# Performance work log

Measured on AMD Instinct MI355X. Metric: run time of the kernel, lower is better.

Reference implementation:

```python
import jax, jax.numpy as jnp
import numpy as np

B, T, N, D = 8, 64, 128, 128  # batch, timesteps, num_nodes, hidden_dim
LN_EPS = 1e-5
L2_EPS = 1e-12


def setup_inputs() -> dict:
    key = jax.random.key(0)
    ks = jax.random.split(key, 8)
    feat = jax.random.normal(ks[0], (B, T, N, D), dtype=jnp.float32)
    w = jax.random.uniform(ks[1], (D,), dtype=jnp.float32)  # learned adj gate (torch.rand init)
    s = 1.0 / np.sqrt(D)
    W1 = jax.random.uniform(ks[2], (D, D), dtype=jnp.float32, minval=-s, maxval=s)
    b1 = jax.random.uniform(ks[3], (D,), dtype=jnp.float32, minval=-s, maxval=s)
    W2 = jax.random.uniform(ks[4], (D, D), dtype=jnp.float32, minval=-s, maxval=s)
    b2 = jax.random.uniform(ks[5], (D,), dtype=jnp.float32, minval=-s, maxval=s)
    gamma = jnp.ones((D,), dtype=jnp.float32)
    beta = jnp.zeros((D,), dtype=jnp.float32)
    return {"feat": feat, "w": w, "W1": W1, "b1": b1, "W2": W2, "b2": b2,
            "gamma": gamma, "beta": beta}


def _windows(x):
    # x: (B, T, N, D) -> (B, T-2, 3*N, D): 3 consecutive timesteps flattened over nodes
    b, t, n, d = x.shape
    return jnp.stack([x[:, i:i + t - 2] for i in range(3)], axis=2).reshape(b, t - 2, 3 * n, d)


def reference(feat, w, W1, b1, W2, b2, gamma, beta):
    # gated + L2-normalized features for learned adjacency
    wf = feat * jax.nn.sigmoid(w)
    wf = wf / jnp.maximum(jnp.linalg.norm(wf, axis=-1, keepdims=True), L2_EPS)

    win = _windows(feat)   # (B, T-2, 3N, D)
    wwin = _windows(wf)    # (B, T-2, 3N, D)

    # learned adjacency: gram matrix per window, (B, T-2, 3N, 3N)
    adj = jnp.einsum('btmd,btnd->btmn', wwin, wwin)

    # symmetric normalization D^{-1/2} A D^{-1/2}; inf/nan (deg<=0) -> 0 as in torch
    deg = adj.sum(axis=-1, keepdims=True)
    dis = jnp.where(deg > 0, jax.lax.rsqrt(jnp.maximum(deg, 1e-38)), 0.0)
    nadj = dis * adj * jnp.swapaxes(dis, -1, -2)

    # message passing, keep last N rows (current timestep)
    agg = jnp.einsum('btmn,btnd->btmd', nadj, win)[:, :, -N:, :]

    # FFN (dropout is identity in eval): Linear -> ReLU -> Linear
    h = jax.nn.relu(agg @ W1 + b1) @ W2 + b2

    # residual with current-timestep features + LayerNorm
    s = feat[:, 2:] + h
    mu = s.mean(axis=-1, keepdims=True)
    var = ((s - mu) ** 2).mean(axis=-1, keepdims=True)
    return (s - mu) * jax.lax.rsqrt(var + LN_EPS) * gamma + beta
```

## Files before the change

### kernel.cpp

```cpp
#include <hip/hip_runtime.h>
#include <math.h>

#define BB    8
#define TDIM  64
#define NN    128
#define DD    128
#define TTOUT 62
#define W3    384
#define LG    136
#define LP    40
#define LW    72

typedef __attribute__((ext_vector_type(8))) short bf16x8;
typedef __attribute__((ext_vector_type(4))) float f32x4;

__device__ __forceinline__ float sigf(float x){ return 1.0f/(1.0f+__expf(-x)); }
__device__ __forceinline__ unsigned short f2bf(float x){
  union{float f; unsigned u;} v; v.f=x;
  unsigned r = v.u + 0x7FFFu + ((v.u>>16)&1u);
  return (unsigned short)(r>>16);
}

__global__ void k_rscale(const float* __restrict__ feat, const float* __restrict__ w,
                         float* __restrict__ rscale){
  int row  = blockIdx.x*4 + (threadIdx.x>>6);
  int lane = threadIdx.x & 63;
  float2 f  = *(const float2*)(feat + (size_t)row*DD + lane*2);
  float2 wv = *(const float2*)(w + lane*2);
  float v0 = f.x * sigf(wv.x);
  float v1 = f.y * sigf(wv.y);
  float ss = v0*v0 + v1*v1;
  #pragma unroll
  for(int k=32;k>=1;k>>=1) ss += __shfl_xor(ss, k);
  if(lane==0) rscale[row] = 1.0f / fmaxf(sqrtf(ss), 1e-12f);
}

__global__ void k_ssum(const float* __restrict__ feat, const float* __restrict__ w,
                       const float* __restrict__ rscale, float* __restrict__ ssum){
  int bt = blockIdx.x;
  int d  = threadIdx.x;
  const float* fp = feat + (size_t)bt*NN*DD + d;
  const float* rp = rscale + bt*NN;
  float acc = 0.f;
  #pragma unroll 4
  for(int n=0;n<NN;n++) acc += fp[(size_t)n*DD] * rp[n];
  ssum[bt*DD + d] = acc * sigf(w[d]);
}

__global__ void k_dis(const float* __restrict__ feat, const float* __restrict__ w,
                      const float* __restrict__ rscale, const float* __restrict__ ssum,
                      float* __restrict__ dis){
  __shared__ float s3[DD];
  __shared__ float sg[DD];
  int bt2 = blockIdx.x;
  int b = bt2 / TTOUT, tt = bt2 % TTOUT;
  int tid = threadIdx.x;
  if(tid < DD){
    int base = (b*TDIM + tt)*DD;
    s3[tid] = ssum[base+tid] + ssum[base+DD+tid] + ssum[base+2*DD+tid];
    sg[tid] = sigf(w[tid]);
  }
  __syncthreads();
  int gr = (b*TDIM + tt)*NN + tid;
  const float4* fr = (const float4*)(feat + (size_t)gr*DD);
  float deg = 0.f;
  #pragma unroll 8
  for(int q=0;q<DD/4;q++){
    float4 f = fr[q];
    deg += f.x*sg[q*4+0]*s3[q*4+0] + f.y*sg[q*4+1]*s3[q*4+1]
         + f.z*sg[q*4+2]*s3[q*4+2] + f.w*sg[q*4+3]*s3[q*4+3];
  }
  deg *= rscale[gr];
  dis[(size_t)bt2*W3 + tid] = (deg > 0.f) ? rsqrtf(fmaxf(deg, 1e-38f)) : 0.f;
}

__global__ __launch_bounds__(512,4) void k_main(
    const float* __restrict__ feat,
    const float* __restrict__ W1, const float* __restrict__ b1,
    const float* __restrict__ W2, const float* __restrict__ b2,
    const float* __restrict__ gamma, const float* __restrict__ beta,
    const float* __restrict__ w,
    const float* __restrict__ rscale, const float* __restrict__ dis,
    float* __restrict__ out)
{
  __shared__ __align__(16) unsigned short sm[32000];
  __shared__ float sSig[DD];
  unsigned short* sA  = sm;
  unsigned short* sG  = sm + 17408;
  unsigned short* sFt = sm + 21760;
  unsigned short* sP  = sm + 26880;
  unsigned short* sWt = sm + 17408;

  const int bt2 = blockIdx.x;
  const int tid = threadIdx.x;
  const int rowBase = (bt2/TTOUT)*TDIM*NN + (bt2%TTOUT)*NN;
  const float* disP = dis + (size_t)bt2*W3;

  const int lane = tid & 63, wid = tid >> 6;
  const int l15 = lane & 15, l4 = lane >> 4;
  const int m0 = wid * 16;

  if(tid < DD) sSig[tid] = sigf(w[tid]);
  __syncthreads();

  #pragma unroll
  for(int e0=0; e0<8; ++e0){
    int e = e0*512 + tid;
    int d = e & 127, r0 = (e>>7)*4;
    float sg = sSig[d];
    #pragma unroll
    for(int i=0;i<4;i++){
      int j = 256 + r0 + i, gr = rowBase + j;
      float f = feat[(size_t)gr*DD + d];
      float fac = rscale[gr]*disP[j];
      sA[(r0+i)*LG + d] = f2bf(f*sg*fac);
    }
  }

  f32x4 acc2[8];
  #pragma unroll
  for(int i=0;i<8;i++) acc2[i] = (f32x4){0.f,0.f,0.f,0.f};

  for(int c=0; c<12; ++c){
    const int n0 = c*32;
    __syncthreads();
    #pragma unroll
    for(int e0=0; e0<2; ++e0){
      int e = e0*512 + tid;
      int d = e & 127, r0 = (e>>7)*4;
      float sg = sSig[d];
      unsigned short fb[4];
      #pragma unroll
      for(int i=0;i<4;i++){
        int j = n0 + r0 + i, gr = rowBase + j;
        float f = feat[(size_t)gr*DD + d];
        float fac = rscale[gr]*disP[j];
        fb[i] = f2bf(f);
        sG[(r0+i)*LG + d] = f2bf(f*sg*fac);
      }
      unsigned int* fp = (unsigned int*)&sFt[d*LP + r0];
      fp[0] = (unsigned)fb[0] | ((unsigned)fb[1]<<16);
      fp[1] = (unsigned)fb[2] | ((unsigned)fb[3]<<16);
    }
    __syncthreads();

    f32x4 p0 = {0.f,0.f,0.f,0.f}, p1 = {0.f,0.f,0.f,0.f};
    #pragma unroll
    for(int ks=0; ks<4; ++ks){
      bf16x8 aA  = *(const bf16x8*)&sA[(m0+l15)*LG + ks*32 + l4*8];
      bf16x8 bg0 = *(const bf16x8*)&sG[( 0+l15)*LG + ks*32 + l4*8];
      bf16x8 bg1 = *(const bf16x8*)&sG[(16+l15)*LG + ks*32 + l4*8];
      p0 = __builtin_amdgcn_mfma_f32_16x16x32_bf16(aA, bg0, p0, 0,0,0);
      p1 = __builtin_amdgcn_mfma_f32_16x16x32_bf16(aA, bg1, p1, 0,0,0);
    }
    #pragma unroll
    for(int r=0;r<4;r++){
      sP[(m0 + l4*4 + r)*LP +  0 + l15] = f2bf(p0[r]);
      sP[(m0 + l4*4 + r)*LP + 16 + l15] = f2bf(p1[r]);
    }
    __syncthreads();

    bf16x8 aP = *(const bf16x8*)&sP[(m0+l15)*LP + l4*8];
    #pragma unroll
    for(int dt=0; dt<8; ++dt){
      bf16x8 bF = *(const bf16x8*)&sFt[(dt*16+l15)*LP + l4*8];
      acc2[dt] = __builtin_amdgcn_mfma_f32_16x16x32_bf16(aP, bF, acc2[dt], 0,0,0);
    }
  }

  #pragma unroll
  for(int dt=0; dt<8; ++dt)
    #pragma unroll
    for(int r=0;r<4;r++)
      sA[(m0+l4*4+r)*LG + dt*16+l15] = f2bf(acc2[dt][r]);

  f32x4 acch[8];
  #pragma unroll
  for(int dt=0; dt<8; ++dt){
    float bv = b1[dt*16+l15];
    acch[dt] = (f32x4){bv,bv,bv,bv};
  }
  for(int kh=0; kh<2; ++kh){
    __syncthreads();
    #pragma unroll
    for(int e0=0; e0<4; ++e0){
      int e = e0*512+tid;
      int n = e&127, k0 = (e>>7)*4;
      float w0 = W1[(size_t)(kh*64+k0+0)*DD + n];
      float w1v= W1[(size_t)(kh*64+k0+1)*DD + n];
      float w2v= W1[(size_t)(kh*64+k0+2)*DD + n];
      float w3v= W1[(size_t)(kh*64+k0+3)*DD + n];
      unsigned int* wp = (unsigned int*)&sWt[n*LW + k0];
      wp[0] = (unsigned)f2bf(w0) | ((unsigned)f2bf(w1v)<<16);
      wp[1] = (unsigned)f2bf(w2v)| ((unsigned)f2bf(w3v)<<16);
    }
    __syncthreads();
    #pragma unroll
    for(int ks=0; ks<2; ++ks){
      bf16x8 aA = *(const bf16x8*)&sA[(m0+l15)*LG + kh*64 + ks*32 + l4*8];
      #pragma unroll
      for(int dt=0; dt<8; ++dt){
        bf16x8 bW = *(const bf16x8*)&sWt[(dt*16+l15)*LW + ks*32 + l4*8];
        acch[dt] = __builtin_amdgcn_mfma_f32_16x16x32_bf16(aA, bW, acch[dt], 0,0,0);
      }
    }
  }
  __syncthreads();
  #pragma unroll
  for(int dt=0; dt<8; ++dt)
    #pragma unroll
    for(int r=0;r<4;r++)
      sA[(m0+l4*4+r)*LG + dt*16+l15] = f2bf(fmaxf(acch[dt][r], 0.f));

  f32x4 acco[8];
  #pragma unroll
  for(int dt=0; dt<8; ++dt){
    float bv = b2[dt*16+l15];
    acco[dt] = (f32x4){bv,bv,bv,bv};
  }
  for(int kh=0; kh<2; ++kh){
    __syncthreads();
    #pragma unroll
    for(int e0=0; e0<4; ++e0){
      int e = e0*512+tid;
      int n = e&127, k0 = (e>>7)*4;
      float w0 = W2[(size_t)(kh*64+k0+0)*DD + n];
      float w1v= W2[(size_t)(kh*64+k0+1)*DD + n];
      float w2v= W2[(size_t)(kh*64+k0+2)*DD + n];
      float w3v= W2[(size_t)(kh*64+k0+3)*DD + n];
      unsigned int* wp = (unsigned int*)&sWt[n*LW + k0];
      wp[0] = (unsigned)f2bf(w0) | ((unsigned)f2bf(w1v)<<16);
      wp[1] = (unsigned)f2bf(w2v)| ((unsigned)f2bf(w3v)<<16);
    }
    __syncthreads();
    #pragma unroll
    for(int ks=0; ks<2; ++ks){
      bf16x8 aA = *(const bf16x8*)&sA[(m0+l15)*LG + kh*64 + ks*32 + l4*8];
      #pragma unroll
      for(int dt=0; dt<8; ++dt){
        bf16x8 bW = *(const bf16x8*)&sWt[(dt*16+l15)*LW + ks*32 + l4*8];
        acco[dt] = __builtin_amdgcn_mfma_f32_16x16x32_bf16(aA, bW, acco[dt], 0,0,0);
      }
    }
  }

  const float* fres = feat + (size_t)(rowBase + 256)*DD;
  #pragma unroll
  for(int r=0;r<4;r++){
    int m = m0 + l4*4 + r;
    float vals[8]; float s1 = 0.f, s2 = 0.f;
    #pragma unroll
    for(int dt=0; dt<8; ++dt){
      int d = dt*16 + l15;
      float v = acco[dt][r] + fres[(size_t)m*DD + d];
      vals[dt] = v; s1 += v; s2 += v*v;
    }
    #pragma unroll
    for(int k=1;k<16;k<<=1){ s1 += __shfl_xor(s1,k); s2 += __shfl_xor(s2,k); }
    float mu   = s1*(1.0f/DD);
    float rstd = rsqrtf(s2*(1.0f/DD) - mu*mu + 1e-5f);
    #pragma unroll
    for(int dt=0; dt<8; ++dt){
      int d = dt*16 + l15;
      out[((size_t)bt2*NN + m)*DD + d] = (vals[dt]-mu)*rstd*gamma[d] + beta[d];
    }
  }
}

extern "C" void kernel_launch(void* const* d_in, const int* in_sizes, int n_in,
                              void* d_out, int out_size, void* d_ws, size_t ws_size,
                              hipStream_t stream){
  const float* feat  = (const float*)d_in[0];
  const float* w     = (const float*)d_in[1];
  const float* W1    = (const float*)d_in[2];
  const float* b1    = (const float*)d_in[3];
  const float* W2    = (const float*)d_in[4];
  const float* b2    = (const float*)d_in[5];
  const float* gamma = (const float*)d_in[6];
  const float* beta  = (const float*)d_in[7];
  float* out = (float*)d_out;

  float* rscale = (float*)d_ws;
  float* ssum   = rscale + BB*TDIM*NN;
  float* dis    = ssum   + BB*TDIM*DD;

  k_rscale<<<BB*TDIM*NN/4, 256, 0, stream>>>(feat, w, rscale);
  k_ssum  <<<BB*TDIM,      128, 0, stream>>>(feat, w, rscale, ssum);
  k_dis   <<<BB*TTOUT,     W3,  0, stream>>>(feat, w, rscale, ssum, dis);
  k_main  <<<BB*TTOUT,     512, 0, stream>>>(feat, W1, b1, W2, b2, gamma, beta, w,
                                             rscale, dis, out);
}
```

Baseline: 90.92 us.

## Fuse prepass kernels, pretranspose weights, double-buffer adjacency chunks in main kernel

Merges the row-norm and column-sum kernels into one pass that also converts W1/W2 into transposed bf16 copies, removing one launch and repeated weight conversion in every block. The main kernel now keeps the current-timestep A tile in registers, caches per-row scale factors in shared memory, and double-buffers the 32-row chunks with register prefetch of the next chunk's features, which cuts one barrier per iteration. It also remaps block IDs for locality and tightens shared-memory padding. The cost is higher register pressure and a heavier shuffle-reduction in the prepass.

```diff
diff --git a/kernel.cpp b/kernel.cpp
--- a/kernel.cpp
+++ b/kernel.cpp
@@ -7,9 +7,10 @@
 #define DD    128
 #define TTOUT 62
 #define W3    384
-#define LG    136
-#define LP    40
-#define LW    72
+#define LA    132
+#define LGS   132
+#define LF    36
+#define LWT   68
 
 typedef __attribute__((ext_vector_type(8))) short bf16x8;
 typedef __attribute__((ext_vector_type(4))) float f32x4;
@@ -21,30 +22,58 @@
   return (unsigned short)(r>>16);
 }
 
-__global__ void k_rscale(const float* __restrict__ feat, const float* __restrict__ w,
-                         float* __restrict__ rscale){
-  int row  = blockIdx.x*4 + (threadIdx.x>>6);
-  int lane = threadIdx.x & 63;
-  float2 f  = *(const float2*)(feat + (size_t)row*DD + lane*2);
-  float2 wv = *(const float2*)(w + lane*2);
-  float v0 = f.x * sigf(wv.x);
-  float v1 = f.y * sigf(wv.y);
-  float ss = v0*v0 + v1*v1;
-  #pragma unroll
-  for(int k=32;k>=1;k>>=1) ss += __shfl_xor(ss, k);
-  if(lane==0) rscale[row] = 1.0f / fmaxf(sqrtf(ss), 1e-12f);
-}
-
-__global__ void k_ssum(const float* __restrict__ feat, const float* __restrict__ w,
-                       const float* __restrict__ rscale, float* __restrict__ ssum){
-  int bt = blockIdx.x;
-  int d  = threadIdx.x;
-  const float* fp = feat + (size_t)bt*NN*DD + d;
-  const float* rp = rscale + bt*NN;
-  float acc = 0.f;
-  #pragma unroll 4
-  for(int n=0;n<NN;n++) acc += fp[(size_t)n*DD] * rp[n];
-  ssum[bt*DD + d] = acc * sigf(w[d]);
+__global__ __launch_bounds__(512) void k_pre(const float* __restrict__ feat,
+    const float* __restrict__ w, const float* __restrict__ W1, const float* __restrict__ W2,
+    float* __restrict__ rscale, float* __restrict__ ssum,
+    unsigned short* __restrict__ W1T, unsigned short* __restrict__ W2T){
+  __shared__ float sSig[DD];
+  __shared__ float sPart[8*DD];
+  const int bid = blockIdx.x, tid = threadIdx.x;
+  if(bid >= BB*TDIM){
+    const float* W = (bid == BB*TDIM) ? W1 : W2;
+    unsigned short* WT = (bid == BB*TDIM) ? W1T : W2T;
+    for(int e=tid; e<DD*DD; e+=512){
+      int k = e>>7, n = e&127;
+      WT[n*DD + k] = f2bf(W[(size_t)k*DD + n]);
+    }
+    return;
+  }
+  const int bt = bid;
+  if(tid < DD) sSig[tid] = sigf(w[tid]);
+  __syncthreads();
+  const int row = tid >> 2, q = tid & 3;
+  const float* fp = feat + ((size_t)bt*NN + row)*DD + q*32;
+  float g[32];
+  #pragma unroll
+  for(int i=0;i<8;i++){
+    float4 v = *(const float4*)(fp + i*4);
+    g[i*4]=v.x; g[i*4+1]=v.y; g[i*4+2]=v.z; g[i*4+3]=v.w;
+  }
+  float ss = 0.f;
+  #pragma unroll
+  for(int j=0;j<32;j++){ g[j] *= sSig[q*32+j]; ss += g[j]*g[j]; }
+  ss += __shfl_xor(ss,1); ss += __shfl_xor(ss,2);
+  float rs = 1.0f / fmaxf(sqrtf(ss), 1e-12f);
+  if(q==0) rscale[(size_t)bt*NN + row] = rs;
+  #pragma unroll
+  for(int j=0;j<32;j++) g[j] *= rs;
+  #pragma unroll
+  for(int k=4;k<64;k<<=1){
+    #pragma unroll
+    for(int j=0;j<32;j++) g[j] += __shfl_xor(g[j], k);
+  }
+  const int lane = tid & 63, wid = tid >> 6;
+  if((lane>>2)==0){
+    #pragma unroll
+    for(int j=0;j<32;j++) sPart[wid*DD + q*32 + j] = g[j];
+  }
+  __syncthreads();
+  if(tid < DD){
+    float s = 0.f;
+    #pragma unroll
+    for(int wv=0; wv<8; wv++) s += sPart[wv*DD + tid];
+    ssum[(size_t)bt*DD + tid] = s;
+  }
 }
 
 __global__ void k_dis(const float* __restrict__ feat, const float* __restrict__ w,
@@ -75,170 +104,197 @@
 }
 
 __global__ __launch_bounds__(512,4) void k_main(
-    const float* __restrict__ feat,
-    const float* __restrict__ W1, const float* __restrict__ b1,
-    const float* __restrict__ W2, const float* __restrict__ b2,
+    const float* __restrict__ feat, const float* __restrict__ w,
+    const float* __restrict__ rscale, const float* __restrict__ dis,
+    const unsigned short* __restrict__ W1T, const float* __restrict__ b1,
+    const unsigned short* __restrict__ W2T, const float* __restrict__ b2,
     const float* __restrict__ gamma, const float* __restrict__ beta,
-    const float* __restrict__ w,
-    const float* __restrict__ rscale, const float* __restrict__ dis,
     float* __restrict__ out)
 {
-  __shared__ __align__(16) unsigned short sm[32000];
-  __shared__ float sSig[DD];
-  unsigned short* sA  = sm;
-  unsigned short* sG  = sm + 17408;
-  unsigned short* sFt = sm + 21760;
-  unsigned short* sP  = sm + 26880;
-  unsigned short* sWt = sm + 17408;
-
-  const int bt2 = blockIdx.x;
-  const int tid = threadIdx.x;
-  const int rowBase = (bt2/TTOUT)*TDIM*NN + (bt2%TTOUT)*NN;
-  const float* disP = dis + (size_t)bt2*W3;
+  __shared__ __align__(16) unsigned short sm[25600];
+  __shared__ __align__(16) float sSig[DD];
+  __shared__ float sFac[W3];
+  unsigned short* sP = sm + 17664;
+
+  const int bid = blockIdx.x, tid = threadIdx.x;
+  const int wg = (bid & 7)*62 + (bid >> 3);
+  const int b = wg / TTOUT, tt = wg % TTOUT;
+  const int rowBase = (b*TDIM + tt)*NN;
+  const float* disP = dis + (size_t)wg*W3;
 
   const int lane = tid & 63, wid = tid >> 6;
   const int l15 = lane & 15, l4 = lane >> 4;
   const int m0 = wid * 16;
 
   if(tid < DD) sSig[tid] = sigf(w[tid]);
-  __syncthreads();
-
-  #pragma unroll
-  for(int e0=0; e0<8; ++e0){
-    int e = e0*512 + tid;
-    int d = e & 127, r0 = (e>>7)*4;
-    float sg = sSig[d];
-    #pragma unroll
-    for(int i=0;i<4;i++){
-      int j = 256 + r0 + i, gr = rowBase + j;
-      float f = feat[(size_t)gr*DD + d];
-      float fac = rscale[gr]*disP[j];
-      sA[(r0+i)*LG + d] = f2bf(f*sg*fac);
-    }
-  }
-
-  f32x4 acc2[8];
-  #pragma unroll
-  for(int i=0;i<8;i++) acc2[i] = (f32x4){0.f,0.f,0.f,0.f};
-
-  for(int c=0; c<12; ++c){
-    const int n0 = c*32;
-    __syncthreads();
+  if(tid < W3) sFac[tid] = rscale[rowBase+tid] * disP[tid];
+  __syncthreads();
+
+  bf16x8 aReg[4];
+  {
+    const float* fr = feat + (size_t)(rowBase + 256 + m0 + l15)*DD;
+    const float fac = sFac[256 + m0 + l15];
+    #pragma unroll
+    for(int ks=0; ks<4; ++ks){
+      float4 v0 = *(const float4*)(fr + ks*32 + l4*8);
+      float4 v1 = *(const float4*)(fr + ks*32 + l4*8 + 4);
+      const float* sg = sSig + ks*32 + l4*8;
+      unsigned short o[8];
+      o[0]=f2bf(v0.x*sg[0]*fac); o[1]=f2bf(v0.y*sg[1]*fac);
+      o[2]=f2bf(v0.z*sg[2]*fac); o[3]=f2bf(v0.w*sg[3]*fac);
+      o[4]=f2bf(v1.x*sg[4]*fac); o[5]=f2bf(v1.y*sg[5]*fac);
+      o[6]=f2bf(v1.z*sg[6]*fac); o[7]=f2bf(v1.w*sg[7]*fac);
+      aReg[ks] = *(bf16x8*)o;
+    }
+  }
+
+  const int d_s = tid & 127, rr = (tid >> 7)*4;
+  float pf[8];
+
+  {
+    #pragma unroll
+    for(int e0=0; e0<2; ++e0)
+      #pragma unroll
+      for(int i=0;i<4;i++)
+        pf[e0*4+i] = feat[(size_t)(rowBase + rr + e0*16 + i)*DD + d_s];
+    unsigned short* sGn  = sm;
+    unsigned short* sFtn = sm + 8448;
+    const float sg = sSig[d_s];
     #pragma unroll
     for(int e0=0; e0<2; ++e0){
-      int e = e0*512 + tid;
-      int d = e & 127, r0 = (e>>7)*4;
-      float sg = sSig[d];
+      const int r0 = rr + e0*16;
       unsigned short fb[4];
       #pragma unroll
       for(int i=0;i<4;i++){
-        int j = n0 + r0 + i, gr = rowBase + j;
-        float f = feat[(size_t)gr*DD + d];
-        float fac = rscale[gr]*disP[j];
+        float f = pf[e0*4+i];
         fb[i] = f2bf(f);
-        sG[(r0+i)*LG + d] = f2bf(f*sg*fac);
-      }
-      unsigned int* fp = (unsigned int*)&sFt[d*LP + r0];
+        sGn[(r0+i)*LGS + d_s] = f2bf(f*sg*sFac[r0+i]);
+      }
+      unsigned* fp = (unsigned*)&sFtn[d_s*LF + r0];
       fp[0] = (unsigned)fb[0] | ((unsigned)fb[1]<<16);
       fp[1] = (unsigned)fb[2] | ((unsigned)fb[3]<<16);
     }
+  }
+  __syncthreads();
+
+  f32x4 acc2[8];
+  #pragma unroll
+  for(int i=0;i<8;i++) acc2[i] = (f32x4){0.f,0.f,0.f,0.f};
+
+  for(int c=0; c<12; ++c){
+    const int pOff = c & 1;
+    const unsigned short* sGc  = sm + pOff*4224;
+    const unsigned short* sFtc = sm + 8448 + pOff*4608;
+    if(c < 11){
+      const int n1 = (c+1)*32;
+      #pragma unroll
+      for(int e0=0; e0<2; ++e0)
+        #pragma unroll
+        for(int i=0;i<4;i++)
+          pf[e0*4+i] = feat[(size_t)(rowBase + n1 + rr + e0*16 + i)*DD + d_s];
+    }
+    f32x4 p0 = {0.f,0.f,0.f,0.f}, p1 = {0.f,0.f,0.f,0.f};
+    #pragma unroll
+    for(int ks=0; ks<4; ++ks){
+      bf16x8 bg0 = *(const bf16x8*)&sGc[( 0+l15)*LGS + ks*32 + l4*8];
+      bf16x8 bg1 = *(const bf16x8*)&sGc[(16+l15)*LGS + ks*32 + l4*8];
+      p0 = __builtin_amdgcn_mfma_f32_16x16x32_bf16(aReg[ks], bg0, p0, 0,0,0);
+      p1 = __builtin_amdgcn_mfma_f32_16x16x32_bf16(aReg[ks], bg1, p1, 0,0,0);
+    }
+    #pragma unroll
+    for(int r=0;r<4;r++){
+      sP[(m0+l4*4+r)*LF +  0 + l15] = f2bf(p0[r]);
+      sP[(m0+l4*4+r)*LF + 16 + l15] = f2bf(p1[r]);
+    }
+    {
+      bf16x8 aP = *(const bf16x8*)&sP[(m0+l15)*LF + l4*8];
+      #pragma unroll
+      for(int dt=0; dt<8; ++dt){
+        bf16x8 bF = *(const bf16x8*)&sFtc[(dt*16+l15)*LF + l4*8];
+        acc2[dt] = __builtin_amdgcn_mfma_f32_16x16x32_bf16(aP, bF, acc2[dt], 0,0,0);
+      }
+    }
+    if(c < 11){
+      unsigned short* sGn  = sm + (pOff^1)*4224;
+      unsigned short* sFtn = sm + 8448 + (pOff^1)*4608;
+      const int n1 = (c+1)*32;
+      const float sg = sSig[d_s];
+      #pragma unroll
+      for(int e0=0; e0<2; ++e0){
+        const int r0 = rr + e0*16;
+        unsigned short fb[4];
+        #pragma unroll
+        for(int i=0;i<4;i++){
+          float f = pf[e0*4+i];
+          fb[i] = f2bf(f);
+          sGn[(r0+i)*LGS + d_s] = f2bf(f*sg*sFac[n1+r0+i]);
+        }
+        unsigned* fp = (unsigned*)&sFtn[d_s*LF + r0];
+        fp[0] = (unsigned)fb[0] | ((unsigned)fb[1]<<16);
+        fp[1] = (unsigned)fb[2] | ((unsigned)fb[3]<<16);
+      }
+    }
     __syncthreads();
-
-    f32x4 p0 = {0.f,0.f,0.f,0.f}, p1 = {0.f,0.f,0.f,0.f};
-    #pragma unroll
-    for(int ks=0; ks<4; ++ks){
-      bf16x8 aA  = *(const bf16x8*)&sA[(m0+l15)*LG + ks*32 + l4*8];
-      bf16x8 bg0 = *(const bf16x8*)&sG[( 0+l15)*LG + ks*32 + l4*8];
-      bf16x8 bg1 = *(const bf16x8*)&sG[(16+l15)*LG + ks*32 + l4*8];
-      p0 = __builtin_amdgcn_mfma_f32_16x16x32_bf16(aA, bg0, p0, 0,0,0);
-      p1 = __builtin_amdgcn_mfma_f32_16x16x32_bf16(aA, bg1, p1, 0,0,0);
-    }
-    #pragma unroll
-    for(int r=0;r<4;r++){
-      sP[(m0 + l4*4 + r)*LP +  0 + l15] = f2bf(p0[r]);
-      sP[(m0 + l4*4 + r)*LP + 16 + l15] = f2bf(p1[r]);
+  }
+
+  unsigned short* ovl = sm;
+  unsigned short* sWt = sm + 16896;
+
+  #pragma unroll
+  for(int dt=0; dt<8; ++dt)
+    #pragma unroll
+    for(int r=0;r<4;r++)
+      ovl[(m0+l4*4+r)*LA + dt*16+l15] = f2bf(acc2[dt][r]);
+
+  f32x4 acch[8];
+  #pragma unroll
+  for(int dt=0; dt<8; ++dt){ float bv = b1[dt*16+l15]; acch[dt] = (f32x4){bv,bv,bv,bv}; }
+  #pragma unroll
+  for(int kh=0; kh<2; ++kh){
+    if(kh) __syncthreads();
+    #pragma unroll
+    for(int it=0; it<2; ++it){
+      int e = it*512 + tid, n = e>>3, sg2 = e&7;
+      uint4 v = *(const uint4*)(W1T + (size_t)n*DD + kh*64 + sg2*8);
+      *(uint4*)(sWt + n*LWT + sg2*8) = v;
     }
     __syncthreads();
-
-    bf16x8 aP = *(const bf16x8*)&sP[(m0+l15)*LP + l4*8];
-    #pragma unroll
-    for(int dt=0; dt<8; ++dt){
-      bf16x8 bF = *(const bf16x8*)&sFt[(dt*16+l15)*LP + l4*8];
-      acc2[dt] = __builtin_amdgcn_mfma_f32_16x16x32_bf16(aP, bF, acc2[dt], 0,0,0);
-    }
-  }
-
+    #pragma unroll
+    for(int ks=0; ks<2; ++ks){
+      bf16x8 aA = *(const bf16x8*)&ovl[(m0+l15)*LA + kh*64 + ks*32 + l4*8];
+      #pragma unroll
+      for(int dt=0; dt<8; ++dt){
+        bf16x8 bW = *(const bf16x8*)&sWt[(dt*16+l15)*LWT + ks*32 + l4*8];
+        acch[dt] = __builtin_amdgcn_mfma_f32_16x16x32_bf16(aA, bW, acch[dt], 0,0,0);
+      }
+    }
+  }
+  __syncthreads();
   #pragma unroll
   for(int dt=0; dt<8; ++dt)
     #pragma unroll
     for(int r=0;r<4;r++)
-      sA[(m0+l4*4+r)*LG + dt*16+l15] = f2bf(acc2[dt][r]);
-
-  f32x4 acch[8];
-  #pragma unroll
-  for(int dt=0; dt<8; ++dt){
-    float bv = b1[dt*16+l15];
-    acch[dt] = (f32x4){bv,bv,bv,bv};
-  }
+      ovl[(m0+l4*4+r)*LA + dt*16+l15] = f2bf(fmaxf(acch[dt][r], 0.f));
+
+  f32x4 acco[8];
+  #pragma unroll
+  for(int dt=0; dt<8; ++dt){ float bv = b2[dt*16+l15]; acco[dt] = (f32x4){bv,bv,bv,bv}; }
+  #pragma unroll
   for(int kh=0; kh<2; ++kh){
+    if(kh) __syncthreads();
+    #pragma unroll
+    for(int it=0; it<2; ++it){
+      int e = it*512 + tid, n = e>>3, sg2 = e&7;
+      uint4 v = *(const uint4*)(W2T + (size_t)n*DD + kh*64 + sg2*8);
+      *(uint4*)(sWt + n*LWT + sg2*8) = v;
+    }
     __syncthreads();
     #pragma unroll
-    for(int e0=0; e0<4; ++e0){
-      int e = e0*512+tid;
-      int n = e&127, k0 = (e>>7)*4;
-      float w0 = W1[(size_t)(kh*64+k0+0)*DD + n];
-      float w1v= W1[(size_t)(kh*64+k0+1)*DD + n];
-      float w2v= W1[(size_t)(kh*64+k0+2)*DD + n];
-      float w3v= W1[(size_t)(kh*64+k0+3)*DD + n];
-      unsigned int* wp = (unsigned int*)&sWt[n*LW + k0];
-      wp[0] = (unsigned)f2bf(w0) | ((unsigned)f2bf(w1v)<<16);
-      wp[1] = (unsigned)f2bf(w2v)| ((unsigned)f2bf(w3v)<<16);
-    }
-    __syncthreads();
-    #pragma unroll
     for(int ks=0; ks<2; ++ks){
-      bf16x8 aA = *(const bf16x8*)&sA[(m0+l15)*LG + kh*64 + ks*32 + l4*8];
+      bf16x8 aA = *(const bf16x8*)&ovl[(m0+l15)*LA + kh*64 + ks*32 + l4*8];
       #pragma unroll
       for(int dt=0; dt<8; ++dt){
-        bf16x8 bW = *(const bf16x8*)&sWt[(dt*16+l15)*LW + ks*32 + l4*8];
-        acch[dt] = __builtin_amdgcn_mfma_f32_16x16x32_bf16(aA, bW, acch[dt], 0,0,0);
-      }
-    }
-  }
-  __syncthreads();
-  #pragma unroll
-  for(int dt=0; dt<8; ++dt)
-    #pragma unroll
-    for(int r=0;r<4;r++)
-      sA[(m0+l4*4+r)*LG + dt*16+l15] = f2bf(fmaxf(acch[dt][r], 0.f));
-
-  f32x4 acco[8];
-  #pragma unroll
-  for(int dt=0; dt<8; ++dt){
-    float bv = b2[dt*16+l15];
-    acco[dt] = (f32x4){bv,bv,bv,bv};
-  }
-  for(int kh=0; kh<2; ++kh){
-    __syncthreads();
-    #pragma unroll
-    for(int e0=0; e0<4; ++e0){
-      int e = e0*512+tid;
-      int n = e&127, k0 = (e>>7)*4;
-      float w0 = W2[(size_t)(kh*64+k0+0)*DD + n];
-      float w1v= W2[(size_t)(kh*64+k0+1)*DD + n];
-      float w2v= W2[(size_t)(kh*64+k0+2)*DD + n];
-      float w3v= W2[(size_t)(kh*64+k0+3)*DD + n];
-      unsigned int* wp = (unsigned int*)&sWt[n*LW + k0];
-      wp[0] = (unsigned)f2bf(w0) | ((unsigned)f2bf(w1v)<<16);
-      wp[1] = (unsigned)f2bf(w2v)| ((unsigned)f2bf(w3v)<<16);
-    }
-    __syncthreads();
-    #pragma unroll
-    for(int ks=0; ks<2; ++ks){
-      bf16x8 aA = *(const bf16x8*)&sA[(m0+l15)*LG + kh*64 + ks*32 + l4*8];
-      #pragma unroll
-      for(int dt=0; dt<8; ++dt){
-        bf16x8 bW = *(const bf16x8*)&sWt[(dt*16+l15)*LW + ks*32 + l4*8];
+        bf16x8 bW = *(const bf16x8*)&sWt[(dt*16+l15)*LWT + ks*32 + l4*8];
         acco[dt] = __builtin_amdgcn_mfma_f32_16x16x32_bf16(aA, bW, acco[dt], 0,0,0);
       }
     }
@@ -262,7 +318,7 @@
     #pragma unroll
     for(int dt=0; dt<8; ++dt){
       int d = dt*16 + l15;
-      out[((size_t)bt2*NN + m)*DD + d] = (vals[dt]-mu)*rstd*gamma[d] + beta[d];
+      out[((size_t)wg*NN + m)*DD + d] = (vals[dt]-mu)*rstd*gamma[d] + beta[d];
     }
   }
 }
@@ -280,13 +336,15 @@
   const float* beta  = (const float*)d_in[7];
   float* out = (float*)d_out;
 
-  float* rscale = (float*)d_ws;
-  float* ssum   = rscale + BB*TDIM*NN;
-  float* dis    = ssum   + BB*TDIM*DD;
-
-  k_rscale<<<BB*TDIM*NN/4, 256, 0, stream>>>(feat, w, rscale);
-  k_ssum  <<<BB*TDIM,      128, 0, stream>>>(feat, w, rscale, ssum);
-  k_dis   <<<BB*TTOUT,     W3,  0, stream>>>(feat, w, rscale, ssum, dis);
-  k_main  <<<BB*TTOUT,     512, 0, stream>>>(feat, W1, b1, W2, b2, gamma, beta, w,
-                                             rscale, dis, out);
-}
+  char* ws = (char*)d_ws;
+  float* rscale = (float*)(ws + 0);
+  float* ssum   = (float*)(ws + 262144);
+  float* dis    = (float*)(ws + 524288);
+  unsigned short* W1T = (unsigned short*)(ws + 1286144);
+  unsigned short* W2T = (unsigned short*)(ws + 1318912);
+
+  k_pre<<<BB*TDIM + 2, 512, 0, stream>>>(feat, w, W1, W2, rscale, ssum, W1T, W2T);
+  k_dis<<<BB*TTOUT, W3, 0, stream>>>(feat, w, rscale, ssum, dis);
+  k_main<<<BB*TTOUT, 512, 0, stream>>>(feat, w, rscale, dis, W1T, b1, W2T, b2,
+                                       gamma, beta, out);
+}
```

Measured after the change: 183.0 us. 2.01x slower.
